# Performance work log

Measured on AMD Instinct MI355X. Metric: run time of the kernel, lower is better.

## Reference

```python
import jax, jax.numpy as jnp
import numpy as np

B, L, D, H = 2, 2048, 512, 8
Dh = D // H


def setup_inputs() -> dict:
    key = jax.random.key(0)
    ks = jax.random.split(key, 12)
    def lin(i):
        W = jax.random.normal(ks[i], (D, D), dtype=jnp.float32) * (1.0 / np.sqrt(D))
        b = jax.random.normal(ks[i + 1], (D,), dtype=jnp.float32) * 0.02
        return W, b
    Wq, bq = lin(0)
    Wk, bk = lin(2)
    Wv, bv = lin(4)
    Wo, bo = lin(6)
    wave_real = jax.random.normal(ks[8], (B, L, D), dtype=jnp.float32)
    wave_imag = jax.random.normal(ks[9], (B, L, D), dtype=jnp.float32)
    return {"wave_real": wave_real, "wave_imag": wave_imag,
            "Wq": Wq, "bq": bq, "Wk": Wk, "bk": bk,
            "Wv": Wv, "bv": bv, "Wo": Wo, "bo": bo}


def _heads(x):
    # (B,L,D) -> (B,H,L,Dh)
    return x.reshape(B, L, H, Dh).transpose(0, 2, 1, 3)


def reference(wave_real, wave_imag, Wq, bq, Wk, bk, Wv, bv, Wo, bo):
    Qr = _heads(wave_real @ Wq.T + bq)
    Qi = _heads(wave_imag @ Wq.T + bq)
    Kr = _heads(wave_real @ Wk.T + bk)
    Ki = _heads(wave_imag @ Wk.T + bk)
    Vr = _heads(wave_real @ Wv.T + bv)
    Vi = _heads(wave_imag @ Wv.T + bv)

    inner_real = jnp.einsum('bhid,bhjd->bhij', Qr, Kr) + jnp.einsum('bhid,bhjd->bhij', Qi, Ki)
    inner_imag = jnp.einsum('bhid,bhjd->bhij', Qr, Ki) - jnp.einsum('bhid,bhjd->bhij', Qi, Kr)

    scores = (inner_real ** 2 + inner_imag ** 2) / np.sqrt(Dh).astype(np.float32)
    attention = jax.nn.softmax(scores, axis=-1)

    phase = jnp.arctan2(inner_imag, inner_real)
    ac = attention * jnp.cos(phase)  # (B,H,L,L)
    as_ = attention * jnp.sin(phase)

    # sum_j att_ij*(Vr_j*cos_ij - Vi_j*sin_ij) -- fused contraction, same math as
    # the original's materialized (B,H,L,L,Dh) rotate-then-sum.
    out_real = jnp.einsum('bhij,bhjd->bhid', ac, Vr) - jnp.einsum('bhij,bhjd->bhid', as_, Vi)
    out_imag = jnp.einsum('bhij,bhjd->bhid', as_, Vr) + jnp.einsum('bhij,bhjd->bhid', ac, Vi)

    out_real = out_real.transpose(0, 2, 1, 3).reshape(B, L, D)
    out_imag = out_imag.transpose(0, 2, 1, 3).reshape(B, L, D)
    return (out_real @ Wo.T + bo, out_imag @ Wo.T + bo, attention)
```

## Files before the change

### kernel.cpp

```cpp
#include <hip/hip_runtime.h>

typedef unsigned short u16;
typedef unsigned int   u32;
typedef __attribute__((ext_vector_type(4)))  u16   us4;
typedef __attribute__((ext_vector_type(8)))  u16   us8;
typedef __attribute__((ext_vector_type(8)))  short s8v;
typedef __attribute__((ext_vector_type(16))) float f32x16;

#define L_   2048
#define D_   512
#define H_   8
#define PE_  2097152ull

#define MATE    2097152ull
#define BHE     131072u
#define VT_OFF  33554432ull
#define ORH_OFF 41943040ull
#define ORL_OFF 46137344ull
#define OIH_OFF 50331648ull
#define OIL_OFF 54525952ull
#define LV_OFF  58720256ull

#define XRH_O 16777216ull
#define XRL_O 20971520ull
#define XIH_O 25165824ull
#define XIL_O 29360128ull
#define WSP_O 33554432ull

#define MFMA32(a,b,c) __builtin_amdgcn_mfma_f32_32x32x16_bf16(a,b,c,0,0,0)
#define ROWOF(r,hi) (((r)&3) + 8*((r)>>2) + 4*(hi))

__device__ __forceinline__ u16 f2bf(float x){
    u32 u = __float_as_uint(x);
    u += 0x7FFFu + ((u>>16)&1u);
    return (u16)(u>>16);
}
__device__ __forceinline__ float bf2f(u16 h){ return __uint_as_float(((u32)h)<<16); }

__device__ __forceinline__ void glds16(const void* gsrc, void* ldst)
{
    __builtin_amdgcn_global_load_lds(
        (const __attribute__((address_space(1))) u32*)(unsigned long long)gsrc,
        (__attribute__((address_space(3))) u32*)(u32)(unsigned long long)ldst,
        16, 0, 0);
}
__device__ __forceinline__ void glds_mat(unsigned char* Lp, u32 matOff,
                                         const u16* g, int rowBase, int lane)
{
    const char* gb = (const char*)(g + (size_t)rowBase * 64);
    #pragma unroll
    for (int s = 0; s < 8; ++s)
        glds16(gb + s*1024 + lane*16, Lp + matOff + s*1024);
}
__device__ __forceinline__ void glds_vt(unsigned char* Lp, u32 matOff,
                                        const u16* g, int j0, int lane, int s0)
{
    #pragma unroll
    for (int s = 0; s < 4; ++s) {
        int seg = s0 + s;
        int dh  = seg*8 + (lane >> 3);
        const char* gp = (const char*)g + (size_t)dh*4096 + (size_t)j0*2 + (lane & 7)*16;
        glds16(gp, Lp + matOff + seg*1024u);
    }
}

__global__ __launch_bounds__(256)
void split_prep_kernel(const float* __restrict__ wr, const float* __restrict__ wi,
                       unsigned char* __restrict__ outb)
{
    const int z = blockIdx.y;
    const float* src = z ? wi : wr;
    u16* hg = (u16*)(outb + (z ? XIH_O : XRH_O));
    u16* lg = (u16*)(outb + (z ? XIL_O : XRL_O));
    const size_t idx4 = ((size_t)blockIdx.x * 256 + threadIdx.x) * 4;
    float4 v = *(const float4*)&src[idx4];
    float vv[4] = { v.x, v.y, v.z, v.w };
    us4 h, l;
    #pragma unroll
    for (int c = 0; c < 4; ++c) {
        u16 hb = f2bf(vv[c]);
        h[c] = hb;
        l[c] = f2bf(vv[c] - bf2f(hb));
    }
    *(us4*)&hg[idx4] = h;
    *(us4*)&lg[idx4] = l;
}

__global__ __launch_bounds__(256)
void wsplit_prep_kernel(const float* __restrict__ Wq, const float* __restrict__ Wk,
                        const float* __restrict__ Wv, unsigned char* __restrict__ outb)
{
    const int tileid = blockIdx.x;
    const int z = blockIdx.y;
    const float* W = (z == 0) ? Wq : (z == 1) ? Wk : Wv;
    u16* hg = (u16*)(outb + WSP_O + (size_t)z*1048576ull) + (size_t)tileid*4096;
    u16* lg = hg + 262144;
    const int nb = tileid >> 3, kb = tileid & 7;
    const int t  = threadIdx.x;
    const int r  = t >> 2;
    const int c0 = (t & 3) * 16;
    const float* src = W + (size_t)(nb*64 + r)*512 + kb*64 + c0;
    #pragma unroll
    for (int j = 0; j < 2; ++j) {
        us8 hv, lv;
        #pragma unroll
        for (int e = 0; e < 8; ++e) {
            float v = src[j*8 + e];
            u16 hb = f2bf(v);
            hv[e] = hb;
            lv[e] = f2bf(v - bf2f(hb));
        }
        int dst = r*64 + ((c0 + j*8) ^ ((r & 7) << 3));
        *(us8*)(hg + dst) = hv;
        *(us8*)(lg + dst) = lv;
    }
}

__device__ __forceinline__ s8v ldfrag(const unsigned char* Lp, u32 matOff, u32 row, u32 colb)
{
    return *(const s8v*)(Lp + matOff + row*128u + (colb ^ ((row&7u)<<4)));
}

__global__ __launch_bounds__(256, 2)
void proj_mfma_kernel(const unsigned char* __restrict__ scr,
                      const float* __restrict__ bq, const float* __restrict__ bk,
                      const float* __restrict__ bv,
                      u16* __restrict__ qk, u16* __restrict__ vt)
{
    const int z = blockIdx.z;
    const u16* Ah_g = (const u16*)(scr + ((z & 1) ? XIH_O : XRH_O));
    const u16* Al_g = (const u16*)(scr + ((z & 1) ? XIL_O : XRL_O));
    const int wsel = z >> 1;
    const float* bias = (wsel == 0) ? bq : (wsel == 1) ? bk : bv;
    const bool four = (wsel < 2);

    const u16* wh = (const u16*)(scr + WSP_O + (size_t)wsel*1048576ull);
    const u16* wl = wh + 262144;

    const int m0 = blockIdx.x * 128;
    const int n0 = blockIdx.y * 64;
    const int nb = blockIdx.y;

    __shared__ __align__(16) unsigned char L[49152];
    enum : u32 { AH=0, AL=16384, BH=32768, BL=40960 };

    const int tid  = threadIdx.x;
    const int lane = tid & 63;
    const int wid  = tid >> 6;
    const int wr   = wid >> 1, wc = wid & 1;
    const int l31  = lane & 31;
    const int hi   = lane >> 5;
    const u32 rowA0 = (u32)(wr*64 + l31);
    const u32 rowB  = (u32)(wc*32 + l31);

    f32x16 c0, c1;
    #pragma unroll
    for (int r = 0; r < 16; ++r) { c0[r] = 0.f; c1[r] = 0.f; }

    const int ch = tid & 7, r0 = tid >> 3;

    for (int k0 = 0; k0 < 512; k0 += 64) {
        __syncthreads();
        {
            const int kb = k0 >> 6;
            const size_t toff = (size_t)(nb*8 + kb)*4096;
            if (wid == 0)              glds_mat(L, BH, wh + toff, 0, lane);
            else if (wid == 1 && four) glds_mat(L, BL, wl + toff, 0, lane);
        }
        #pragma unroll
        for (int rr = 0; rr < 4; ++rr) {
            u32 row = (u32)(rr*32 + r0);
            u32 dst = row*128u + (((u32)ch<<4) ^ ((row&7u)<<4));
            us8 vh = *(const us8*)(Ah_g + (size_t)(m0 + row)*512 + k0 + ch*8);
            *(us8*)(L + AH + dst) = vh;
            if (four) {
                us8 vl = *(const us8*)(Al_g + (size_t)(m0 + row)*512 + k0 + ch*8);
                *(us8*)(L + AL + dst) = vl;
            }
        }
        __syncthreads();

        #pragma unroll
        for (int ks = 0; ks < 4; ++ks) {
            u32 colb = (u32)(ks*32 + hi*16);
            s8v a0h = ldfrag(L, AH, rowA0,      colb);
            s8v a1h = ldfrag(L, AH, rowA0 + 32, colb);
            s8v bh_ = ldfrag(L, BH, rowB,       colb);
            c0 = MFMA32(a0h, bh_, c0);
            c1 = MFMA32(a1h, bh_, c1);
            if (four) {
                s8v a0l = ldfrag(L, AL, rowA0,      colb);
                s8v a1l = ldfrag(L, AL, rowA0 + 32, colb);
                s8v bl_ = ldfrag(L, BL, rowB,       colb);
                c0 = MFMA32(a0h, bl_, c0); c0 = MFMA32(a0l, bh_, c0); c0 = MFMA32(a0l, bl_, c0);
                c1 = MFMA32(a1h, bl_, c1); c1 = MFMA32(a1l, bh_, c1); c1 = MFMA32(a1l, bl_, c1);
            }
        }
    }

    const int n  = n0 + wc*32 + l31;
    const float bvv = bias[n];
    const int h  = n >> 6, dh = n & 63;

    if (z < 4) {
        u16* hg = qk + (size_t)(2*z)   * MATE;
        u16* lg = qk + (size_t)(2*z+1) * MATE;
        #pragma unroll
        for (int f = 0; f < 2; ++f) {
            const f32x16& c = f ? c1 : c0;
            #pragma unroll
            for (int r = 0; r < 16; ++r) {
                int m  = m0 + wr*64 + 32*f + ROWOF(r, hi);
                int b_ = m >> 11, i = m & 2047;
                size_t idx = (size_t)(b_*8 + h)*BHE + (size_t)i*64 + (dh ^ ((i&7)<<3));
                float v = c[r] + bvv;
                u16 hb = f2bf(v);
                hg[idx] = hb;
                lg[idx] = f2bf(v - bf2f(hb));
            }
        }
    } else {
        u16* vg = vt + (size_t)(z & 1) * MATE;
        #pragma unroll
        for (int f = 0; f < 2; ++f) {
            const f32x16& c = f ? c1 : c0;
            #pragma unroll
            for (int g = 0; g < 4; ++g) {
                int mb = m0 + wr*64 + 32*f + 8*g + 4*hi;
                int b_ = mb >> 11, ib = mb & 2047;
                us4 pv;
                #pragma unroll
                for (int j = 0; j < 4; ++j) pv[j] = f2bf(c[4*g + j] + bvv);
                int ibs = ib ^ ((dh & 7) << 3);
                *(us4*)&vg[(size_t)(b_*8 + h)*BHE + (size_t)dh*2048 + ibs] = pv;
            }
        }
    }
}

__global__ __launch_bounds__(256, 2)
void attn_mfma_kernel(const u16* __restrict__ qk,
                      const u16* __restrict__ vt,
                      float* __restrict__ attnbuf,
                      u16* __restrict__ orh, u16* __restrict__ orl,
                      u16* __restrict__ oih, u16* __restrict__ oil,
                      float* __restrict__ l_out)
{
    const int bid = blockIdx.x;
    const int xcd = bid & 7;
    const int seq = bid >> 3;
    const int bh  = xcd*2 + (seq >> 5);
    const int i0  = (seq & 31) * 64;
    const int tid  = threadIdx.x;
    const int lane = tid & 63;
    const int wid  = tid >> 6;
    const int wr   = wid >> 1, wc = wid & 1;
    const int l31  = lane & 31;
    const int hi   = lane >> 5;
    const u32 rowA = wr*32 + l31;
    const u32 rowB = wc*32 + l31;

    __shared__ __align__(16) unsigned char L[49152];
    enum : u32 { QRH=0, QIH=8192,
                 KRH=16384, KRL=24576, KIH=32768, KIL=40960,
                 VRo=16384, VIo=24576,
                 PAC=32768, PAS=40960 };
    float* sc = (float*)(L + PAC);

    const u16* qrh = qk + 0*MATE + (size_t)bh*BHE;
    const u16* qrl = qk + 1*MATE + (size_t)bh*BHE;
    const u16* qih = qk + 2*MATE + (size_t)bh*BHE;
    const u16* qil = qk + 3*MATE + (size_t)bh*BHE;
    const u16* krh = qk + 4*MATE + (size_t)bh*BHE;
    const u16* krl = qk + 5*MATE + (size_t)bh*BHE;
    const u16* kih = qk + 6*MATE + (size_t)bh*BHE;
    const u16* kil = qk + 7*MATE + (size_t)bh*BHE;
    const u16* vtr = vt + 0*MATE + (size_t)bh*BHE;
    const u16* vti = vt + 1*MATE + (size_t)bh*BHE;

    {
        const u16* qsrc = (wid == 0) ? qrh : (wid == 1) ? qih : (wid == 2) ? qrl : qil;
        const u32  qdst = (wid == 0) ? QRH : (wid == 1) ? QIH : (wid == 2) ? KRH : KRL;
        glds_mat(L, qdst, qsrc, i0, lane);
    }
    __syncthreads();
    s8v qfl[2][4];
    #pragma unroll
    for (int ks = 0; ks < 4; ++ks) {
        u32 colb = (u32)(ks*32 + hi*16);
        qfl[0][ks] = ldfrag(L, KRH, rowA, colb);
        qfl[1][ks] = ldfrag(L, KRL, rowA, colb);
    }

    float mxv[16];
    #pragma unroll
    for (int r = 0; r < 16; ++r) mxv[r] = 0.f;

    const u16* s1src = (wid & 1) ? kih : krh;
    const u32  s1off = 16384u + (u32)wid * 8192u;

    for (int jp = 0; jp < 16; ++jp) {
        __syncthreads();
        glds_mat(L, s1off, s1src, (2*jp + (wid >> 1))*64, lane);
        __syncthreads();
        __builtin_amdgcn_s_setprio(1);
        #pragma unroll
        for (int half = 0; half < 2; ++half) {
            const u32 kR = half ? KIH : KRH;
            const u32 kI = half ? KIL : KRL;
            f32x16 ir, ip, in_;
            #pragma unroll
            for (int r = 0; r < 16; ++r) { ir[r]=0.f; ip[r]=0.f; in_[r]=0.f; }
            #pragma unroll
            for (int ks = 0; ks < 4; ++ks) {
                u32 colb = ks*32 + hi*16;
                s8v aR = ldfrag(L, QRH, rowA, colb);
                s8v aI = ldfrag(L, QIH, rowA, colb);
                s8v bR = ldfrag(L, kR,  rowB, colb);
                s8v bI = ldfrag(L, kI,  rowB, colb);
                ir  = MFMA32(aR, bR, ir);
                ir  = MFMA32(aI, bI, ir);
                ip  = MFMA32(aR, bI, ip);
                in_ = MFMA32(aI, bR, in_);
            }
            #pragma unroll
            for (int r = 0; r < 16; ++r) {
                float xr = ir[r], xi = ip[r] - in_[r];
                float q = xr*xr + xi*xi;
                mxv[r] = fmaxf(mxv[r], q * 0.125f);
            }
        }
        __builtin_amdgcn_s_setprio(0);
    }
    #pragma unroll
    for (int m = 1; m < 32; m <<= 1)
        #pragma unroll
        for (int r = 0; r < 16; ++r) mxv[r] = fmaxf(mxv[r], __shfl_xor(mxv[r], m));

    __syncthreads();
    #pragma unroll
    for (int r = 0; r < 16; ++r)
        if (l31 == r) sc[wc*64 + wr*32 + ROWOF(r,hi)] = mxv[r];
    __syncthreads();
    float mfin[16];
    #pragma unroll
    for (int r = 0; r < 16; ++r) {
        u32 row = wr*32 + ROWOF(r,hi);
        mfin[r] = fmaxf(sc[row], sc[64 + row]);
    }

    f32x16 ore, oim;
    float lp[16];
    #pragma unroll
    for (int r = 0; r < 16; ++r) { ore[r]=0.f; oim[r]=0.f; lp[r]=0.f; }

    const u16* s2src = (wid == 0) ? krh : (wid == 1) ? krl : (wid == 2) ? kih : kil;
    const u32  s2off = 16384u + (u32)wid * 8192u;
    const u16* vsrc  = (wid < 2) ? vtr : vti;
    const u32  voff  = (wid < 2) ? VRo : VIo;
    const int  vseg  = (wid & 1) * 4;

    u16* ebase = (u16*)(attnbuf + (size_t)bh*4194304ull + (size_t)i0*2048);

    for (int jt = 0; jt < 32; ++jt) {
        const int j0 = jt * 64;
        __syncthreads();
        glds_mat(L, s2off, s2src, j0, lane);
        __syncthreads();

        f32x16 ir, ip, in_;
        #pragma unroll
        for (int r = 0; r < 16; ++r) { ir[r]=0.f; ip[r]=0.f; in_[r]=0.f; }
        __builtin_amdgcn_s_setprio(1);
        #pragma unroll
        for (int ks = 0; ks < 4; ++ks) {
            u32 colb = ks*32 + hi*16;
            s8v aRH = ldfrag(L, QRH, rowA, colb);
            s8v aIH = ldfrag(L, QIH, rowA, colb);
            s8v aRL = qfl[0][ks];
            s8v aIL = qfl[1][ks];
            s8v bRH = ldfrag(L, KRH, rowB, colb);
            s8v bRL = ldfrag(L, KRL, rowB, colb);
            s8v bIH = ldfrag(L, KIH, rowB, colb);
            s8v bIL = ldfrag(L, KIL, rowB, colb);
            ir = MFMA32(aRH, bRH, ir); ir = MFMA32(aRH, bRL, ir); ir = MFMA32(aRL, bRH, ir);
            ir = MFMA32(aIH, bIH, ir); ir = MFMA32(aIH, bIL, ir); ir = MFMA32(aIL, bIH, ir);
            ip  = MFMA32(aRH, bIH, ip);  ip  = MFMA32(aRH, bIL, ip);  ip  = MFMA32(aRL, bIH, ip);
            in_ = MFMA32(aIH, bRH, in_); in_ = MFMA32(aIH, bRL, in_); in_ = MFMA32(aIL, bRH, in_);
        }
        __builtin_amdgcn_s_setprio(0);
        __syncthreads();

        glds_vt(L, voff, vsrc, j0, lane, vseg);

        #pragma unroll
        for (int r = 0; r < 16; ++r) {
            float xr = ir[r], xi = ip[r] - in_[r];
            float q  = fmaf(xr, xr, xi*xi);
            float e  = __expf(fmaf(q, 0.125f, -mfin[r]));
            lp[r] += e;
            float iv = rsqrtf(q);
            float t  = e * iv;
            float pc = (q > 0.f) ? xr*t : e;
            float ps = (q > 0.f) ? xi*t : 0.0f;
            u32 rowloc = wr*32 + ROWOF(r,hi);
            ebase[(size_t)rowloc*4096 + j0 + wc*32 + l31] = f2bf(e);
            u32 colb2 = (wc*32 + l31)*2;
            *(u16*)(L + PAC + rowloc*128u + (colb2 ^ ((rowloc&7u)<<4))) = f2bf(pc);
            *(u16*)(L + PAS + rowloc*128u + (colb2 ^ ((rowloc&7u)<<4))) = f2bf(ps);
        }
        __syncthreads();

        __builtin_amdgcn_s_setprio(1);
        #pragma unroll
        for (int ks = 0; ks < 4; ++ks) {
            u32 colb = ks*32 + hi*16;
            s8v aC = ldfrag(L, PAC, rowA, colb);
            s8v aS = ldfrag(L, PAS, rowA, colb);
            s8v vR = ldfrag(L, VRo, rowB, colb);
            s8v vI = ldfrag(L, VIo, rowB, colb);
            s8v vN = vI ^ (short)0x8000;
            ore = MFMA32(aC, vR, ore); ore = MFMA32(aS, vN, ore);
            oim = MFMA32(aS, vR, oim); oim = MFMA32(aC, vI, oim);
        }
        __builtin_amdgcn_s_setprio(0);
    }

    #pragma unroll
    for (int m = 1; m < 32; m <<= 1)
        #pragma unroll
        for (int r = 0; r < 16; ++r) lp[r] += __shfl_xor(lp[r], m);

    __syncthreads();
    #pragma unroll
    for (int r = 0; r < 16; ++r)
        if (l31 == r) sc[wc*64 + wr*32 + ROWOF(r,hi)] = lp[r];
    __syncthreads();

    const int b_ = bh >> 3, h = bh & 7;
    const size_t cb = (size_t)h*64 + wc*32 + l31;
    #pragma unroll
    for (int r = 0; r < 16; ++r) {
        u32 row = wr*32 + ROWOF(r,hi);
        float ls = sc[row] + sc[64 + row];
        if (wc == 0 && l31 == 0) l_out[(size_t)bh*2048 + i0 + row] = ls;
        float inv = 1.0f / ls;
        size_t idx = ((size_t)b_*2048 + i0 + row)*512 + cb;
        float vr = ore[r] * inv;
        float vi = oim[r] * inv;
        u16 hr = f2bf(vr); orh[idx] = hr; orl[idx] = f2bf(vr - bf2f(hr));
        u16 hw = f2bf(vi); oih[idx] = hw; oil[idx] = f2bf(vi - bf2f(hw));
    }
}

__global__ __launch_bounds__(256)
void expand_attn_kernel(float* __restrict__ attnbuf, const float* __restrict__ l)
{
    const int row = blockIdx.x;
    const float inv = 1.f / l[row];
    float* rowf = attnbuf + (size_t)row * 2048;
    const us8 ev = *(const us8*)((const u16*)rowf + threadIdx.x * 8);
    __syncthreads();
    float4 o0, o1;
    o0.x = bf2f(ev[0])*inv; o0.y = bf2f(ev[1])*inv;
    o0.z = bf2f(ev[2])*inv; o0.w = bf2f(ev[3])*inv;
    o1.x = bf2f(ev[4])*inv; o1.y = bf2f(ev[5])*inv;
    o1.z = bf2f(ev[6])*inv; o1.w = bf2f(ev[7])*inv;
    float* dst = rowf + threadIdx.x * 8;
    *(float4*)dst       = o0;
    *(float4*)(dst + 4) = o1;
}

__global__ __launch_bounds__(256, 2)
void oproj_mfma_kernel(const unsigned char* __restrict__ wsb,
                       const float* __restrict__ Wo, const float* __restrict__ bo,
                       float* __restrict__ out)
{
    const int z = blockIdx.z;
    const u16* Ah_g = (const u16*)(wsb + (z ? OIH_OFF : ORH_OFF));
    const u16* Al_g = (const u16*)(wsb + (z ? OIL_OFF : ORL_OFF));
    float* outp = out + (size_t)z * PE_;

    const int m0 = blockIdx.x * 128;
    const int n0 = blockIdx.y * 64;

    __shared__ __align__(16) unsigned char L[49152];
    enum : u32 { AH=0, AL=16384, BH=32768, BL=40960 };

    const int tid  = threadIdx.x;
    const int lane = tid & 63;
    const int wid  = tid >> 6;
    const int wr   = wid >> 1, wc = wid & 1;
    const int l31  = lane & 31;
    const int hi   = lane >> 5;
    const u32 rowA0 = (u32)(wr*64 + l31);
    const u32 rowB  = (u32)(wc*32 + l31);

    f32x16 c0, c1;
    #pragma unroll
    for (int r = 0; r < 16; ++r) { c0[r] = 0.f; c1[r] = 0.f; }

    const int ch = tid & 7, r0 = tid >> 3;

    for (int k0 = 0; k0 < 512; k0 += 64) {
        __syncthreads();
        #pragma unroll
        for (int rr = 0; rr < 4; ++rr) {
            u32 row = (u32)(rr*32 + r0);
            u32 dst = row*128u + (((u32)ch<<4) ^ ((row&7u)<<4));
            us8 vh = *(const us8*)(Ah_g + (size_t)(m0 + row)*512 + k0 + ch*8);
            us8 vl = *(const us8*)(Al_g + (size_t)(m0 + row)*512 + k0 + ch*8);
            *(us8*)(L + AH + dst) = vh;
            *(us8*)(L + AL + dst) = vl;
        }
        #pragma unroll
        for (int rr = 0; rr < 2; ++rr) {
            u32 row = (u32)(rr*32 + r0);
            const float* src = Wo + (size_t)(n0 + row)*512 + k0 + ch*8;
            float4 v0 = *(const float4*)src;
            float4 v1 = *(const float4*)(src + 4);
            float vv[8] = { v0.x,v0.y,v0.z,v0.w, v1.x,v1.y,v1.z,v1.w };
            us8 hv, lv;
            #pragma unroll
            for (int j = 0; j < 8; ++j) {
                u16 hb = f2bf(vv[j]);
                hv[j] = hb;
                lv[j] = f2bf(vv[j] - bf2f(hb));
            }
            u32 dst = row*128u + (((u32)ch<<4) ^ ((row&7u)<<4));
            *(us8*)(L + BH + dst) = hv;
            *(us8*)(L + BL + dst) = lv;
        }
        __syncthreads();

        #pragma unroll
        for (int ks = 0; ks < 4; ++ks) {
            u32 colb = (u32)(ks*32 + hi*16);
            s8v a0h = ldfrag(L, AH, rowA0,      colb);
            s8v a1h = ldfrag(L, AH, rowA0 + 32, colb);
            s8v a0l = ldfrag(L, AL, rowA0,      colb);
            s8v a1l = ldfrag(L, AL, rowA0 + 32, colb);
            s8v bh_ = ldfrag(L, BH, rowB,       colb);
            s8v bl_ = ldfrag(L, BL, rowB,       colb);
            c0 = MFMA32(a0h, bh_, c0); c0 = MFMA32(a0h, bl_, c0); c0 = MFMA32(a0l, bh_, c0);
            c1 = MFMA32(a1h, bh_, c1); c1 = MFMA32(a1h, bl_, c1); c1 = MFMA32(a1l, bh_, c1);
        }
    }

    const int n = n0 + wc*32 + l31;
    const float bvv = bo[n];
    #pragma unroll
    for (int f = 0; f < 2; ++f) {
        const f32x16& c = f ? c1 : c0;
        #pragma unroll
        for (int r = 0; r < 16; ++r) {
            int m = m0 + wr*64 + 32*f + ROWOF(r, hi);
            outp[(size_t)m*512 + n] = c[r] + bvv;
        }
    }
}

extern "C" void kernel_launch(void* const* d_in, const int* in_sizes, int n_in,
                              void* d_out, int out_size, void* d_ws, size_t ws_size,
                              hipStream_t stream)
{
    const float* wave_real = (const float*)d_in[0];
    const float* wave_imag = (const float*)d_in[1];
    const float* Wq = (const float*)d_in[2]; const float* bq = (const float*)d_in[3];
    const float* Wk = (const float*)d_in[4]; const float* bk = (const float*)d_in[5];
    const float* Wv = (const float*)d_in[6]; const float* bv = (const float*)d_in[7];
    const float* Wo = (const float*)d_in[8]; const float* bo = (const float*)d_in[9];
    float* out = (float*)d_out;
    unsigned char* outb = (unsigned char*)d_out;
    unsigned char* wsb  = (unsigned char*)d_ws;

    float* attnbuf = out + 2*PE_;

    split_prep_kernel<<<dim3(2048, 2), dim3(256), 0, stream>>>(wave_real, wave_imag, outb);

    wsplit_prep_kernel<<<dim3(64, 3), dim3(256), 0, stream>>>(Wq, Wk, Wv, outb);

    proj_mfma_kernel<<<dim3(32, 8, 6), dim3(256), 0, stream>>>(
        outb, bq, bk, bv,
        (u16*)wsb, (u16*)(wsb + VT_OFF));

    attn_mfma_kernel<<<dim3(512), dim3(256), 0, stream>>>(
        (const u16*)wsb, (const u16*)(wsb + VT_OFF), attnbuf,
        (u16*)(wsb + ORH_OFF), (u16*)(wsb + ORL_OFF),
        (u16*)(wsb + OIH_OFF), (u16*)(wsb + OIL_OFF),
        (float*)(wsb + LV_OFF));

    expand_attn_kernel<<<dim3(32768), dim3(256), 0, stream>>>(
        attnbuf, (const float*)(wsb + LV_OFF));

    oproj_mfma_kernel<<<dim3(32, 8, 2), dim3(256), 0, stream>>>(
        wsb, Wo, bo, out);
}
```

Measured before the change: 331.3 us.

## Split row-max pass into separate kernel parallelized over key halves

Moves the first pass of the attention kernel, which computes the per-row maximum of the scores, into its own kernel. That kernel launches 1024 blocks, each covering half of the key range, and writes two partial maxima per row to workspace. The attention kernel then reads and combines these maxima instead of computing them. The intent is to get more parallelism than the 512-block grid offers for the max pass, at the cost of an extra launch and reloading Q fragments.

```diff
diff --git a/kernel.cpp b/kernel.cpp
--- a/kernel.cpp
+++ b/kernel.cpp
@@ -20,6 +20,8 @@
 #define OIH_OFF 50331648ull
 #define OIL_OFF 54525952ull
 #define LV_OFF  58720256ull
+#define MX0_OFF 58851328ull
+#define MX1_OFF 58982400ull
 
 #define XRH_O 16777216ull
 #define XRL_O 20971520ull
@@ -239,18 +241,17 @@
 }
 
 __global__ __launch_bounds__(256, 2)
-void attn_mfma_kernel(const u16* __restrict__ qk,
-                      const u16* __restrict__ vt,
-                      float* __restrict__ attnbuf,
-                      u16* __restrict__ orh, u16* __restrict__ orl,
-                      u16* __restrict__ oih, u16* __restrict__ oil,
-                      float* __restrict__ l_out)
+void qkmax_kernel(const u16* __restrict__ qk,
+                  float* __restrict__ mx0, float* __restrict__ mx1)
 {
     const int bid = blockIdx.x;
     const int xcd = bid & 7;
     const int seq = bid >> 3;
-    const int bh  = xcd*2 + (seq >> 5);
-    const int i0  = (seq & 31) * 64;
+    const int bh  = xcd*2 + (seq >> 6);
+    const int rem = seq & 63;
+    const int i0  = (rem >> 1) * 64;
+    const int jh  = rem & 1;
+    const int jbase = jh * 16;
     const int tid  = threadIdx.x;
     const int lane = tid & 63;
     const int wid  = tid >> 6;
@@ -261,53 +262,33 @@
     const u32 rowB = wc*32 + l31;
 
     __shared__ __align__(16) unsigned char L[49152];
-    enum : u32 { QRH=0, QIH=8192,
-                 KRH=16384, KRL=24576, KIH=32768, KIL=40960,
-                 VRo=16384, VIo=24576,
-                 PAC=32768, PAS=40960 };
-    float* sc = (float*)(L + PAC);
+    enum : u32 { QRH=0, QIH=8192, KB0=16384 };
+    float* sc = (float*)(L + KB0);
 
     const u16* qrh = qk + 0*MATE + (size_t)bh*BHE;
-    const u16* qrl = qk + 1*MATE + (size_t)bh*BHE;
     const u16* qih = qk + 2*MATE + (size_t)bh*BHE;
-    const u16* qil = qk + 3*MATE + (size_t)bh*BHE;
     const u16* krh = qk + 4*MATE + (size_t)bh*BHE;
-    const u16* krl = qk + 5*MATE + (size_t)bh*BHE;
     const u16* kih = qk + 6*MATE + (size_t)bh*BHE;
-    const u16* kil = qk + 7*MATE + (size_t)bh*BHE;
-    const u16* vtr = vt + 0*MATE + (size_t)bh*BHE;
-    const u16* vti = vt + 1*MATE + (size_t)bh*BHE;
-
-    {
-        const u16* qsrc = (wid == 0) ? qrh : (wid == 1) ? qih : (wid == 2) ? qrl : qil;
-        const u32  qdst = (wid == 0) ? QRH : (wid == 1) ? QIH : (wid == 2) ? KRH : KRL;
-        glds_mat(L, qdst, qsrc, i0, lane);
-    }
-    __syncthreads();
-    s8v qfl[2][4];
-    #pragma unroll
-    for (int ks = 0; ks < 4; ++ks) {
-        u32 colb = (u32)(ks*32 + hi*16);
-        qfl[0][ks] = ldfrag(L, KRH, rowA, colb);
-        qfl[1][ks] = ldfrag(L, KRL, rowA, colb);
-    }
+
+    if (wid == 0)      glds_mat(L, QRH, qrh, i0, lane);
+    else if (wid == 1) glds_mat(L, QIH, qih, i0, lane);
 
     float mxv[16];
     #pragma unroll
     for (int r = 0; r < 16; ++r) mxv[r] = 0.f;
 
     const u16* s1src = (wid & 1) ? kih : krh;
-    const u32  s1off = 16384u + (u32)wid * 8192u;
-
-    for (int jp = 0; jp < 16; ++jp) {
-        __syncthreads();
-        glds_mat(L, s1off, s1src, (2*jp + (wid >> 1))*64, lane);
+    const u32  s1off = KB0 + (u32)wid * 8192u;
+
+    for (int jp = 0; jp < 8; ++jp) {
+        __syncthreads();
+        glds_mat(L, s1off, s1src, (jbase + 2*jp + (wid >> 1))*64, lane);
         __syncthreads();
         __builtin_amdgcn_s_setprio(1);
         #pragma unroll
         for (int half = 0; half < 2; ++half) {
-            const u32 kR = half ? KIH : KRH;
-            const u32 kI = half ? KIL : KRL;
+            const u32 kR = KB0 + (half ? 16384u : 0u);
+            const u32 kI = kR + 8192u;
             f32x16 ir, ip, in_;
             #pragma unroll
             for (int r = 0; r < 16; ++r) { ir[r]=0.f; ip[r]=0.f; in_[r]=0.f; }
@@ -342,11 +323,75 @@
     for (int r = 0; r < 16; ++r)
         if (l31 == r) sc[wc*64 + wr*32 + ROWOF(r,hi)] = mxv[r];
     __syncthreads();
+
+    if (tid < 64) {
+        float* gout = (jh ? mx1 : mx0) + (size_t)bh*2048 + i0;
+        gout[tid] = fmaxf(sc[tid], sc[64 + tid]);
+    }
+}
+
+__global__ __launch_bounds__(256, 2)
+void attn_mfma_kernel(const u16* __restrict__ qk,
+                      const u16* __restrict__ vt,
+                      float* __restrict__ attnbuf,
+                      u16* __restrict__ orh, u16* __restrict__ orl,
+                      u16* __restrict__ oih, u16* __restrict__ oil,
+                      float* __restrict__ l_out,
+                      const float* __restrict__ mx0, const float* __restrict__ mx1)
+{
+    const int bid = blockIdx.x;
+    const int xcd = bid & 7;
+    const int seq = bid >> 3;
+    const int bh  = xcd*2 + (seq >> 5);
+    const int i0  = (seq & 31) * 64;
+    const int tid  = threadIdx.x;
+    const int lane = tid & 63;
+    const int wid  = tid >> 6;
+    const int wr   = wid >> 1, wc = wid & 1;
+    const int l31  = lane & 31;
+    const int hi   = lane >> 5;
+    const u32 rowA = wr*32 + l31;
+    const u32 rowB = wc*32 + l31;
+
+    __shared__ __align__(16) unsigned char L[49152];
+    enum : u32 { QRH=0, QIH=8192,
+                 KRH=16384, KRL=24576, KIH=32768, KIL=40960,
+                 VRo=16384, VIo=24576,
+                 PAC=32768, PAS=40960 };
+    float* sc = (float*)(L + PAC);
+
+    const u16* qrh = qk + 0*MATE + (size_t)bh*BHE;
+    const u16* qrl = qk + 1*MATE + (size_t)bh*BHE;
+    const u16* qih = qk + 2*MATE + (size_t)bh*BHE;
+    const u16* qil = qk + 3*MATE + (size_t)bh*BHE;
+    const u16* krh = qk + 4*MATE + (size_t)bh*BHE;
+    const u16* krl = qk + 5*MATE + (size_t)bh*BHE;
+    const u16* kih = qk + 6*MATE + (size_t)bh*BHE;
+    const u16* kil = qk + 7*MATE + (size_t)bh*BHE;
+    const u16* vtr = vt + 0*MATE + (size_t)bh*BHE;
+    const u16* vti = vt + 1*MATE + (size_t)bh*BHE;
+
+    {
+        const u16* qsrc = (wid == 0) ? qrh : (wid == 1) ? qih : (wid == 2) ? qrl : qil;
+        const u32  qdst = (wid == 0) ? QRH : (wid == 1) ? QIH : (wid == 2) ? KRH : KRL;
+        glds_mat(L, qdst, qsrc, i0, lane);
+    }
+    __syncthreads();
+    s8v qfl[2][4];
+    #pragma unroll
+    for (int ks = 0; ks < 4; ++ks) {
+        u32 colb = (u32)(ks*32 + hi*16);
+        qfl[0][ks] = ldfrag(L, KRH, rowA, colb);
+        qfl[1][ks] = ldfrag(L, KRL, rowA, colb);
+    }
+
+    const float* m0b = mx0 + (size_t)bh*2048 + i0;
+    const float* m1b = mx1 + (size_t)bh*2048 + i0;
     float mfin[16];
     #pragma unroll
     for (int r = 0; r < 16; ++r) {
         u32 row = wr*32 + ROWOF(r,hi);
-        mfin[r] = fmaxf(sc[row], sc[64 + row]);
+        mfin[r] = fmaxf(m0b[row], m1b[row]);
     }
 
     f32x16 ore, oim;
@@ -584,11 +629,15 @@
         outb, bq, bk, bv,
         (u16*)wsb, (u16*)(wsb + VT_OFF));
 
+    qkmax_kernel<<<dim3(1024), dim3(256), 0, stream>>>(
+        (const u16*)wsb, (float*)(wsb + MX0_OFF), (float*)(wsb + MX1_OFF));
+
     attn_mfma_kernel<<<dim3(512), dim3(256), 0, stream>>>(
         (const u16*)wsb, (const u16*)(wsb + VT_OFF), attnbuf,
         (u16*)(wsb + ORH_OFF), (u16*)(wsb + ORL_OFF),
         (u16*)(wsb + OIH_OFF), (u16*)(wsb + OIL_OFF),
-        (float*)(wsb + LV_OFF));
+        (float*)(wsb + LV_OFF),
+        (const float*)(wsb + MX0_OFF), (const float*)(wsb + MX1_OFF));
 
     expand_attn_kernel<<<dim3(32768), dim3(256), 0, stream>>>(
         attnbuf, (const float*)(wsb + LV_OFF));
```

Result: slower. 343.0 us (+3.5%).
